# Optimization experiments

Hardware: AMD Instinct MI355X
Metric: run time of the kernel (lower is better)

Reference implementation:

```python
import jax, jax.numpy as jnp
import numpy as np

H, MEL, ATT, TXT = 1024, 80, 640, 640   # n_hidden, n_mel, n_attn_channels, n_text+n_speaker
T, TTXT = 600, 128


def setup_inputs() -> dict:
    key = jax.random.key(0)
    ks = jax.random.split(key, 20)
    def w(k, shape, s=0.02):
        return (jax.random.normal(k, shape) * s).astype(jnp.float32)
    return {
        "residual": jax.random.normal(ks[0], (T, 1, MEL), jnp.float32),
        "text": jax.random.normal(ks[1], (TTXT, 1, TXT), jnp.float32),
        # attention_lstm: LSTM(MEL -> H), 1 layer
        "Wih_a": w(ks[2], (4 * H, MEL)), "Whh_a": w(ks[3], (4 * H, H)),
        "bih_a": jnp.zeros(4 * H, jnp.float32), "bhh_a": jnp.zeros(4 * H, jnp.float32),
        # Attention: query/key/value projections + scoring vector v
        "Wq": w(ks[4], (ATT, H)), "Wk": w(ks[5], (ATT, TXT)), "Wv": w(ks[6], (ATT, TXT)),
        "v_w": w(ks[7], (ATT,)),
        # decoder lstm: LSTM(H+ATT -> H), 2 layers
        "Wih0": w(ks[8], (4 * H, H + ATT)), "Whh0": w(ks[9], (4 * H, H)),
        "bih0": jnp.zeros(4 * H, jnp.float32), "bhh0": jnp.zeros(4 * H, jnp.float32),
        "Wih1": w(ks[10], (4 * H, H)), "Whh1": w(ks[11], (4 * H, H)),
        "bih1": jnp.zeros(4 * H, jnp.float32), "bhh1": jnp.zeros(4 * H, jnp.float32),
        # DenseLayer: two tanh(Linear(H,H))
        "D0w": w(ks[12], (H, H)), "D0b": jnp.zeros(H, jnp.float32),
        "D1w": w(ks[13], (H, H)), "D1b": jnp.zeros(H, jnp.float32),
        # Conv1d(H, 2*MEL, kernel=1) == Linear
        "conv_w": w(ks[14], (2 * MEL, H)), "conv_b": jnp.zeros(2 * MEL, jnp.float32),
        # gate layer: Linear(H+ATT, 1)
        "gate_w": w(ks[15], (H + ATT,)), "gate_b": jnp.zeros((), jnp.float32),
    }


def lstm_cell(x, h, c, Wih, Whh, bih, bhh):
    # PyTorch gate order: i, f, g, o
    g = Wih @ x + bih + Whh @ h + bhh
    i, f, gg, o = jnp.split(g, 4)
    c2 = jax.nn.sigmoid(f) * c + jax.nn.sigmoid(i) * jnp.tanh(gg)
    return jax.nn.sigmoid(o) * jnp.tanh(c2), c2


def ar_back_step(residual, text, Wih_a, Whh_a, bih_a, bhh_a, Wq, Wk, Wv, v_w,
                 Wih0, Whh0, bih0, bhh0, Wih1, Whh1, bih1, bhh1,
                 D0w, D0b, D1w, D1b, conv_w, conv_b, gate_w, gate_b):
    res = residual[::-1, 0, :]            # AR_Back_Step flips time; batch=1 squeezed
    txt = text[:, 0, :]                   # [TTXT, TXT]
    K = txt @ Wk.T                        # [TTXT, ATT]  (keys constant over steps)
    V = txt @ Wv.T                        # [TTXT, ATT]
    z = jnp.zeros(H, jnp.float32)
    carry0 = (jnp.zeros(MEL, jnp.float32), z, z, z, z, z, z)

    def step(carry, r_t):
        out_prev, h, c, h0, c0, h1, c1 = carry
        # attention LSTM on previous output
        h, c = lstm_cell(out_prev, h, c, Wih_a, Whh_a, bih_a, bhh_a)
        # additive (Bahdanau-style) attention: v . tanh(q + K)
        q = Wq @ h                                   # [ATT]
        scores = jnp.tanh(q[None, :] + K) @ v_w      # [TTXT]
        attn = jax.nn.softmax(scores)
        ctx = attn @ V                               # [ATT]
        dec_in = jnp.concatenate([h, ctx])           # [H+ATT]
        # 2-layer decoder LSTM
        h0, c0 = lstm_cell(dec_in, h0, c0, Wih0, Whh0, bih0, bhh0)
        h1, c1 = lstm_cell(h0, h1, c1, Wih1, Whh1, bih1, bhh1)
        # DenseLayer (tanh MLP) then 1x1 conv
        d = jnp.tanh(D1w @ jnp.tanh(D0w @ h1 + D0b) + D1b)
        dec_out = conv_w @ d + conv_b                # [2*MEL]
        log_s, b = dec_out[:MEL], dec_out[MEL:]
        out = (r_t - b) / jnp.exp(log_s)             # affine coupling inverse
        gate = jax.nn.sigmoid(gate_w @ dec_in + gate_b)
        return (out, h, c, h0, c0, h1, c1), (out, gate)

    _, (outs, gates) = jax.lax.scan(step, carry0, res)
    total = outs[::-1][:, None, :]                   # flip back, restore batch dim
    return total, gates


def reference(residual, text, Wih_a, Whh_a, bih_a, bhh_a, Wq, Wk, Wv, v_w,
              Wih0, Whh0, bih0, bhh0, Wih1, Whh1, bih1, bhh1,
              D0w, D0b, D1w, D1b, conv_w, conv_b, gate_w, gate_b):
    return ar_back_step(residual, text, Wih_a, Whh_a, bih_a, bhh_a, Wq, Wk, Wv, v_w,
                        Wih0, Whh0, bih0, bhh0, Wih1, Whh1, bih1, bhh1,
                        D0w, D0b, D1w, D1b, conv_w, conv_b, gate_w, gate_b)
```

## Files before the change

### kernel.cpp

```cpp
#include <hip/hip_runtime.h>

#define NBLK 256
#define NTHR 1024

constexpr int H = 1024, MEL = 80, ATT = 640, TXTD = 640, T = 600, TTXT = 128;
constexpr int G4 = 4096, DIN = H + ATT;

constexpr int WS_K     = 0;
constexpr int WS_V     = WS_K + TTXT * ATT;
constexpr int WS_HV    = WS_V + TTXT * ATT;
constexpr int WS_H0V   = WS_HV + H;
constexpr int WS_H1V   = WS_H0V + H;
constexpr int WS_Q     = WS_H1V + H;
constexpr int WS_SV    = WS_Q + ATT;
constexpr int WS_DEN   = WS_SV + ATT;
constexpr int WS_GH    = WS_DEN + 1;
constexpr int WS_DEC   = (WS_GH + 1 + 15) & ~15;
constexpr int WS_A0    = (WS_DEC + 2 * MEL + 15) & ~15;
constexpr int WS_END   = WS_A0 + H;
constexpr int WS_BAR   = (WS_END + 63) & ~63;

constexpr int SM_W0  = 0;
constexpr int SM_H   = SM_W0 + 16 * DIN;
constexpr int SM_H0  = SM_H + H;
constexpr int SM_H1  = SM_H0 + H;
constexpr int SM_A0  = SM_H1 + H;
constexpr int SM_ATT = SM_A0 + H;
constexpr int SM_K   = SM_ATT + ATT;
constexpr int SM_V   = SM_K + ATT;
constexpr int SM_VW  = SM_V + ATT;
constexpr int SM_OUT = SM_VW + ATT;
constexpr int SM_DEC = SM_OUT + MEL;
constexpr int SM_RED = SM_DEC + 2 * MEL;
constexpr int SM_D   = SM_RED + 16;
constexpr int SM_M   = SM_D + 4;
constexpr int SM_MG  = SM_M + 16 * TTXT;
constexpr int SM_SV  = SM_MG + TTXT;
constexpr int SM_CNT = SM_SV + TTXT;
constexpr size_t SM_BYTES = ((size_t)SM_CNT * 4 + 255) & ~(size_t)255;

#define KEEP4(v) \
  asm volatile("" : "+v"((v).x), "+v"((v).y), "+v"((v).z), "+v"((v).w))

struct Params {
  const float *residual, *text, *Wih_a, *Whh_a, *bih_a, *bhh_a,
      *Wq, *Wk, *Wv, *v_w, *Wih0, *Whh0, *bih0, *bhh0,
      *Wih1, *Whh1, *bih1, *bhh1, *D0w, *D0b, *D1w, *D1b,
      *conv_w, *conv_b, *gate_w, *gate_b;
  float* out;
  float* ws;
};

__device__ __forceinline__ float sigm(float x) { return 1.0f / (1.0f + __expf(-x)); }
__device__ __forceinline__ float ftanh(float x) {
  x = fminf(15.f, fmaxf(-15.f, x));
  float e = __expf(2.f * x);
  return (e - 1.f) / (e + 1.f);
}

__device__ __forceinline__ float aload(const float* p) {
  return __hip_atomic_load(p, __ATOMIC_RELAXED, __HIP_MEMORY_SCOPE_AGENT);
}
__device__ __forceinline__ void astore(float* p, float v) {
  __hip_atomic_store(p, v, __ATOMIC_RELAXED, __HIP_MEMORY_SCOPE_AGENT);
}

__device__ __forceinline__ void g_arrive(unsigned* bar) {
  asm volatile("s_waitcnt vmcnt(0)" ::: "memory");
  __syncthreads();
  if (threadIdx.x == 0) {
    unsigned* leaf = bar + (blockIdx.x & 15) * 32;
    unsigned o = __hip_atomic_fetch_add(leaf, 1u, __ATOMIC_RELAXED,
                                        __HIP_MEMORY_SCOPE_AGENT);
    if ((o & 15) == 15)
      __hip_atomic_fetch_add(bar + 544, 1u, __ATOMIC_RELAXED,
                             __HIP_MEMORY_SCOPE_AGENT);
  }
}
__device__ __forceinline__ void g_wait(unsigned* bar, unsigned target) {
  if (threadIdx.x == 0) {
    while (__hip_atomic_load(bar + 544, __ATOMIC_RELAXED,
                             __HIP_MEMORY_SCOPE_AGENT) < target)
      __builtin_amdgcn_s_sleep(1);
  }
  __syncthreads();
}

__device__ __forceinline__ float red64(float s) {
#pragma unroll
  for (int off = 32; off; off >>= 1) s += __shfl_xor(s, off, 64);
  return s;
}

__device__ __forceinline__ float dot16pin(float4 w0, float4 w1, float4 w2,
                                          float4 w3, const float* x, int lane) {
  const float4* x4 = (const float4*)x;
  float4 b0 = x4[lane], b1 = x4[lane + 64], b2 = x4[lane + 128],
         b3 = x4[lane + 192];
  float s0 = w0.x * b0.x, s1 = w1.x * b1.x;
  s0 = fmaf(w0.y, b0.y, s0); s1 = fmaf(w1.y, b1.y, s1);
  s0 = fmaf(w0.z, b0.z, s0); s1 = fmaf(w1.z, b1.z, s1);
  s0 = fmaf(w0.w, b0.w, s0); s1 = fmaf(w1.w, b1.w, s1);
  s0 = fmaf(w2.x, b2.x, s0); s1 = fmaf(w3.x, b3.x, s1);
  s0 = fmaf(w2.y, b2.y, s0); s1 = fmaf(w3.y, b3.y, s1);
  s0 = fmaf(w2.z, b2.z, s0); s1 = fmaf(w3.z, b3.z, s1);
  s0 = fmaf(w2.w, b2.w, s0); s1 = fmaf(w3.w, b3.w, s1);
  return s0 + s1;
}

__device__ __forceinline__ float dot16load(const float* w, const float* x,
                                           int lane) {
  const float4* w4 = (const float4*)w;
  const float4* x4 = (const float4*)x;
  float4 a0 = w4[lane], a1 = w4[lane + 64], a2 = w4[lane + 128],
         a3 = w4[lane + 192];
  float4 b0 = x4[lane], b1 = x4[lane + 64], b2 = x4[lane + 128],
         b3 = x4[lane + 192];
  float s0 = a0.x * b0.x, s1 = a1.x * b1.x;
  s0 = fmaf(a0.y, b0.y, s0); s1 = fmaf(a1.y, b1.y, s1);
  s0 = fmaf(a0.z, b0.z, s0); s1 = fmaf(a1.z, b1.z, s1);
  s0 = fmaf(a0.w, b0.w, s0); s1 = fmaf(a1.w, b1.w, s1);
  s0 = fmaf(a2.x, b2.x, s0); s1 = fmaf(a3.x, b3.x, s1);
  s0 = fmaf(a2.y, b2.y, s0); s1 = fmaf(a3.y, b3.y, s1);
  s0 = fmaf(a2.z, b2.z, s0); s1 = fmaf(a3.z, b3.z, s1);
  s0 = fmaf(a2.w, b2.w, s0); s1 = fmaf(a3.w, b3.w, s1);
  return s0 + s1;
}

__device__ __forceinline__ float wave_dot(const float* __restrict__ w,
                                          const float* __restrict__ x,
                                          int n4, int lane) {
  float s = 0.f;
  const float4* w4 = (const float4*)w;
  const float4* x4 = (const float4*)x;
  for (int i = lane; i < n4; i += 64) {
    float4 a = w4[i];
    float4 b = x4[i];
    s = fmaf(a.x, b.x, s);
    s = fmaf(a.y, b.y, s);
    s = fmaf(a.z, b.z, s);
    s = fmaf(a.w, b.w, s);
  }
  return red64(s);
}

__global__ void __launch_bounds__(NTHR, 4) ar_kernel(Params p) {
  const int b = blockIdx.x;
  const int tid = threadIdx.x;
  const int wave = tid >> 6;
  const int lane = tid & 63;
  const int sg = wave >> 2;
  const int wg = wave & 3;
  const int gw = b * 16 + wave;

  float* ws = p.ws;
  float* Kw = ws + WS_K;
  float* Vw = ws + WS_V;
  float* hv = ws + WS_HV;
  float* h0v = ws + WS_H0V;
  float* h1v = ws + WS_H1V;
  float* qv = ws + WS_Q;
  float* sv = ws + WS_SV;
  float* ghp = ws + WS_GH;
  float* dec = ws + WS_DEC;
  float* a0g = ws + WS_A0;
  unsigned* bar = (unsigned*)(ws + WS_BAR);

  extern __shared__ __align__(16) float smem[];
  float* s_w0 = smem + SM_W0;
  float* s_h = smem + SM_H;
  float* s_h0 = smem + SM_H0;
  float* s_h1 = smem + SM_H1;
  float* s_a0 = smem + SM_A0;
  float* s_att = smem + SM_ATT;
  float* s_k = smem + SM_K;
  float* s_v = smem + SM_V;
  float* s_vw = smem + SM_VW;
  float* s_out = smem + SM_OUT;
  float* s_dec = smem + SM_DEC;
  float* s_red = smem + SM_RED;
  float* s_d = smem + SM_D;
  float* s_m = smem + SM_M;
  float* s_mg = smem + SM_MG;
  float* s_sv = smem + SM_SV;

  const int e = 4 * b + sg;
  const int grow = e + wg * H;

  const float4* WA = (const float4*)(p.Whh_a + (size_t)grow * H);
  float4 wa0 = WA[lane], wa1 = WA[lane + 64], wa2 = WA[lane + 128],
         wa3 = WA[lane + 192];
  KEEP4(wa0); KEEP4(wa1); KEEP4(wa2); KEEP4(wa3);
  const float4* W0 = (const float4*)(p.Whh0 + (size_t)grow * H);
  float4 w00 = W0[lane], w01 = W0[lane + 64], w02 = W0[lane + 128],
         w03 = W0[lane + 192];
  KEEP4(w00); KEEP4(w01); KEEP4(w02); KEEP4(w03);
  const float4* W1 = (const float4*)(p.Whh1 + (size_t)grow * H);
  float4 w10 = W1[lane], w11 = W1[lane + 64], w12 = W1[lane + 128],
         w13 = W1[lane + 192];
  KEEP4(w10); KEEP4(w11); KEEP4(w12); KEEP4(w13);
  const float4* WI = (const float4*)(p.Wih1 + (size_t)grow * H);
  float4 wi0 = WI[lane], wi1 = WI[lane + 64], wi2 = WI[lane + 128],
         wi3 = WI[lane + 192];
  KEEP4(wi0); KEEP4(wi1); KEEP4(wi2); KEEP4(wi3);
  float4 wma = make_float4(0.f, 0.f, 0.f, 0.f);
  if (lane < MEL / 4)
    wma = ((const float4*)(p.Wih_a + (size_t)grow * MEL))[lane];
  KEEP4(wma);
  float4 wf = ((const float4*)(p.D0w + (size_t)e * H))[wg * 64 + lane];
  KEEP4(wf);
  float4 wgd = ((const float4*)(p.D1w + (size_t)e * H))[wg * 64 + lane];
  KEEP4(wgd);
  float4 wcv = make_float4(0.f, 0.f, 0.f, 0.f);
  if (tid < 2 * MEL) wcv = ((const float4*)(p.conv_w + (size_t)tid * H))[b];
  KEEP4(wcv);
  const float ba = p.bih_a[grow] + p.bhh_a[grow];
  const float b0s = p.bih0[grow] + p.bhh0[grow];
  const float b1s = p.bih1[grow] + p.bhh1[grow];

  const float* xsrc = nullptr;
  if (gw < ATT) xsrc = p.Wq + (size_t)gw * H;
  else if (gw == ATT) xsrc = p.gate_w;

  {
    const float4* src = (const float4*)(p.Wih0 + (size_t)grow * DIN);
    float4* dst = (float4*)(s_w0 + wave * DIN);
    for (int i = lane; i < DIN / 4; i += 64) dst[i] = src[i];
  }
  for (int i = tid; i < ATT; i += NTHR) s_vw[i] = p.v_w[i];
  s_h[tid] = 0.f;
  s_h0[tid] = 0.f;
  s_h1[tid] = 0.f;

  float c_reg = 0.f, c0_reg = 0.f, c1_reg = 0.f;
  float u0_reg = 0.f, u1_reg = 0.f, w0h_reg = 0.f;

  unsigned bk = 0;

  for (int idx = gw; idx < 2 * TTXT * ATT; idx += NBLK * 16) {
    int isV = idx >= TTXT * ATT;
    int rem = isV ? idx - TTXT * ATT : idx;
    int j = rem / ATT;
    int a = rem - j * ATT;
    const float* wrow = (isV ? p.Wv : p.Wk) + a * TXTD;
    float s = wave_dot(wrow, p.text + j * TXTD, TXTD / 4, lane);
    if (lane == 0) astore(&(isV ? Vw : Kw)[j * ATT + a], s);
  }
  g_arrive(bar); ++bk; g_wait(bar, 16 * bk);
  if (b < TTXT) {
    for (int i = tid; i < ATT; i += NTHR) {
      s_k[i] = aload(&Kw[b * ATT + i]);
      s_v[i] = aload(&Vw[b * ATT + i]);
    }
  }
  {
    const float4* wrow = (const float4*)(s_w0 + wave * DIN + H);
    for (int j = 0; j < TTXT; ++j) {
      const float4* v4 = (const float4*)(Vw + j * ATT);
      float s = 0.f;
      for (int i = lane; i < ATT / 4; i += 64) {
        float4 a = wrow[i], x = v4[i];
        s = fmaf(a.x, x.x, s);
        s = fmaf(a.y, x.y, s);
        s = fmaf(a.z, x.z, s);
        s = fmaf(a.w, x.w, s);
      }
      s = red64(s);
      if (lane == 0) s_m[wave * TTXT + j] = s;
    }
  }
  if (b == 0) {
    for (int j = wave; j < TTXT; j += 16) {
      float s = wave_dot(p.gate_w + H, Vw + j * ATT, ATT / 4, lane);
      if (lane == 0) s_mg[j] = s;
    }
  }
  __syncthreads();

  for (int t = 0; t < T; ++t) {
    if (tid < 2 * MEL) s_dec[tid] = aload(dec + tid);
    __syncthreads();
    if (tid < MEL) {
      float o = 0.f;
      if (t != 0) {
        float ls = s_dec[tid] + p.conv_b[tid];
        float bb = s_dec[MEL + tid] + p.conv_b[MEL + tid];
        float r = p.residual[(T - t) * MEL + tid];
        o = (r - bb) * __expf(-ls);
        if (b == 0) p.out[(T - t) * MEL + tid] = o;
      }
      s_out[tid] = o;
    }
    __syncthreads();
    {
      float pa = dot16pin(wa0, wa1, wa2, wa3, s_h, lane);
      if (lane < MEL / 4) {
        float4 bm = ((const float4*)s_out)[lane];
        pa = fmaf(wma.x, bm.x, pa);
        pa = fmaf(wma.y, bm.y, pa);
        pa = fmaf(wma.z, bm.z, pa);
        pa = fmaf(wma.w, bm.w, pa);
      }
      pa = red64(pa);
      if (lane == 0) s_red[wave] = pa + ba;
      __syncthreads();
      if (tid < 4) {
        int ee = 4 * b + tid;
        float gi = s_red[tid * 4 + 0], gf = s_red[tid * 4 + 1];
        float gg = s_red[tid * 4 + 2], go = s_red[tid * 4 + 3];
        float c2 = sigm(gf) * c_reg + sigm(gi) * ftanh(gg);
        c_reg = c2;
        astore(&hv[ee], sigm(go) * ftanh(c2));
      }
    }
    g_arrive(bar); ++bk;
    g_wait(bar, 16 * bk);

    s_h[tid] = aload(hv + tid);
    __syncthreads();
    if (xsrc) {
      float q = dot16load(xsrc, s_h, lane);
      q = red64(q);
      if (lane == 0) {
        if (gw < ATT) astore(&qv[gw], q);
        else astore(&ghp[0], q);
      }
    }
    if (b == NBLK - 1) {
      for (int i = tid; i < 2 * MEL; i += NTHR) astore(&dec[i], 0.f);
    }
    g_arrive(bar); ++bk;
    w0h_reg = red64(dot16load(s_w0 + wave * DIN, s_h, lane));
    g_wait(bar, 16 * bk);

    if (b < TTXT) {
      if (tid < ATT) s_att[tid] = aload(&qv[tid]);
      __syncthreads();
      float sp = 0.f;
      for (int i = tid; i < ATT; i += NTHR)
        sp += ftanh(s_att[i] + s_k[i]) * s_vw[i];
      sp = red64(sp);
      if (lane == 0) s_red[wave] = sp;
      __syncthreads();
      if (tid == 0) {
        float sc = 0.f;
#pragma unroll
        for (int k = 0; k < 16; ++k) sc += s_red[k];
        astore(&sv[b], sc);
      }
    }
    g_arrive(bar); ++bk;
    g_wait(bar, 16 * bk);

    {
      if (tid < TTXT) s_sv[tid] = aload(&sv[tid]);
      __syncthreads();
      float pa_ = __expf(s_sv[lane] - 16.f);
      float pb_ = __expf(s_sv[lane + 64] - 16.f);
      float den_ = red64(pa_ + pb_);
      float w0c = red64(fmaf(pa_, s_m[wave * TTXT + lane],
                             pb_ * s_m[wave * TTXT + lane + 64]));
      if (lane == 0) s_red[wave] = w0c / den_ + w0h_reg + u0_reg + b0s;
      __syncthreads();
      if (tid < 4) {
        int ee = 4 * b + tid;
        float gi = s_red[tid * 4 + 0], gf = s_red[tid * 4 + 1];
        float gg = s_red[tid * 4 + 2], go = s_red[tid * 4 + 3];
        float c2 = sigm(gf) * c0_reg + sigm(gi) * ftanh(gg);
        c0_reg = c2;
        astore(&h0v[ee], sigm(go) * ftanh(c2));
      }
    }
    g_arrive(bar); ++bk;
    if (b == 0 && wave == 15) {
      float pa_ = __expf(s_sv[lane] - 16.f);
      float pb_ = __expf(s_sv[lane + 64] - 16.f);
      float den_ = red64(pa_ + pb_);
      float gc = red64(fmaf(pa_, s_mg[lane], pb_ * s_mg[lane + 64]));
      if (lane == 0) {
        float gh = aload(&ghp[0]);
        p.out[T * MEL + t] = sigm(gh + gc / den_ + p.gate_b[0]);
      }
    }
    g_wait(bar, 16 * bk);

    s_h0[tid] = aload(h0v + tid);
    __syncthreads();
    {
      float pe = dot16pin(wi0, wi1, wi2, wi3, s_h0, lane);
      pe = red64(pe);
      if (lane == 0) s_red[wave] = pe + u1_reg + b1s;
      __syncthreads();
      if (tid < 4) {
        int ee = 4 * b + tid;
        float gi = s_red[tid * 4 + 0], gf = s_red[tid * 4 + 1];
        float gg = s_red[tid * 4 + 2], go = s_red[tid * 4 + 3];
        float c2 = sigm(gf) * c1_reg + sigm(gi) * ftanh(gg);
        c1_reg = c2;
        astore(&h1v[ee], sigm(go) * ftanh(c2));
      }
    }
    g_arrive(bar); ++bk;
    u0_reg = red64(dot16pin(w00, w01, w02, w03, s_h0, lane));
    g_wait(bar, 16 * bk);

    s_h1[tid] = aload(h1v + tid);
    __syncthreads();
    {
      float4 x = ((const float4*)s_h1)[wg * 64 + lane];
      float s = wf.x * x.x;
      s = fmaf(wf.y, x.y, s); s = fmaf(wf.z, x.z, s); s = fmaf(wf.w, x.w, s);
      s = red64(s);
      if (lane == 0) s_red[wave] = s;
      __syncthreads();
      if (tid < 4) {
        int r2 = 4 * b + tid;
        float tot = s_red[tid * 4] + s_red[tid * 4 + 1] + s_red[tid * 4 + 2] +
                    s_red[tid * 4 + 3];
        astore(&a0g[r2], ftanh(tot + p.D0b[r2]));
      }
    }
    g_arrive(bar); ++bk;
    u1_reg = red64(dot16pin(w10, w11, w12, w13, s_h1, lane));
    g_wait(bar, 16 * bk);

    s_a0[tid] = aload(a0g + tid);
    __syncthreads();
    {
      float4 x = ((const float4*)s_a0)[wg * 64 + lane];
      float s = wgd.x * x.x;
      s = fmaf(wgd.y, x.y, s); s = fmaf(wgd.z, x.z, s); s = fmaf(wgd.w, x.w, s);
      s = red64(s);
      if (lane == 0) s_red[wave] = s;
      __syncthreads();
      if (tid < 4) {
        int r2 = 4 * b + tid;
        float tot = s_red[tid * 4] + s_red[tid * 4 + 1] + s_red[tid * 4 + 2] +
                    s_red[tid * 4 + 3];
        s_d[tid] = ftanh(tot + p.D1b[r2]);
      }
      __syncthreads();
      if (tid < 2 * MEL) {
        float acc = wcv.x * s_d[0];
        acc = fmaf(wcv.y, s_d[1], acc);
        acc = fmaf(wcv.z, s_d[2], acc);
        acc = fmaf(wcv.w, s_d[3], acc);
        atomicAdd(&dec[tid], acc);
      }
    }
    g_arrive(bar); ++bk;
    g_wait(bar, 16 * bk);
  }

  if (b == 0 && tid < MEL) {
    float ls = aload(&dec[tid]) + p.conv_b[tid];
    float bb = aload(&dec[MEL + tid]) + p.conv_b[MEL + tid];
    float r = p.residual[tid];
    p.out[tid] = (r - bb) * __expf(-ls);
  }
}

extern "C" void kernel_launch(void* const* d_in, const int* in_sizes, int n_in,
                              void* d_out, int out_size, void* d_ws, size_t ws_size,
                              hipStream_t stream) {
  Params hp;
  hp.residual = (const float*)d_in[0];
  hp.text = (const float*)d_in[1];
  hp.Wih_a = (const float*)d_in[2];
  hp.Whh_a = (const float*)d_in[3];
  hp.bih_a = (const float*)d_in[4];
  hp.bhh_a = (const float*)d_in[5];
  hp.Wq = (const float*)d_in[6];
  hp.Wk = (const float*)d_in[7];
  hp.Wv = (const float*)d_in[8];
  hp.v_w = (const float*)d_in[9];
  hp.Wih0 = (const float*)d_in[10];
  hp.Whh0 = (const float*)d_in[11];
  hp.bih0 = (const float*)d_in[12];
  hp.bhh0 = (const float*)d_in[13];
  hp.Wih1 = (const float*)d_in[14];
  hp.Whh1 = (const float*)d_in[15];
  hp.bih1 = (const float*)d_in[16];
  hp.bhh1 = (const float*)d_in[17];
  hp.D0w = (const float*)d_in[18];
  hp.D0b = (const float*)d_in[19];
  hp.D1w = (const float*)d_in[20];
  hp.D1b = (const float*)d_in[21];
  hp.conv_w = (const float*)d_in[22];
  hp.conv_b = (const float*)d_in[23];
  hp.gate_w = (const float*)d_in[24];
  hp.gate_b = (const float*)d_in[25];
  hp.out = (float*)d_out;
  hp.ws = (float*)d_ws;

  hipMemsetAsync((char*)d_ws + (size_t)WS_BAR * sizeof(float), 0, 4096, stream);

  void* args[] = {&hp};
  hipLaunchCooperativeKernel((void*)ar_kernel, dim3(NBLK), dim3(NTHR), args,
                             (uint32_t)SM_BYTES, stream);
}
```

Before: 25.47 ms.

## Fuse query projection and attention scoring to drop a grid barrier per step

Each of the first 128 blocks now computes five query rows locally and immediately scores all text positions against its slice of K. Partial scores are accumulated with atomics into eight striped buffers, which removes the separate query-to-global exchange and one grid-wide barrier per timestep. The striped buffers are zeroed by the last block later in the step, before they are reused. In exchange it adds atomic traffic, spreads the score sum across blocks, and changes the floating-point summation order.

```diff
diff --git a/kernel.cpp b/kernel.cpp
--- a/kernel.cpp
+++ b/kernel.cpp
@@ -5,16 +5,15 @@
 
 constexpr int H = 1024, MEL = 80, ATT = 640, TXTD = 640, T = 600, TTXT = 128;
 constexpr int G4 = 4096, DIN = H + ATT;
+constexpr int QPB = 5;
 
 constexpr int WS_K     = 0;
 constexpr int WS_V     = WS_K + TTXT * ATT;
 constexpr int WS_HV    = WS_V + TTXT * ATT;
 constexpr int WS_H0V   = WS_HV + H;
 constexpr int WS_H1V   = WS_H0V + H;
-constexpr int WS_Q     = WS_H1V + H;
-constexpr int WS_SV    = WS_Q + ATT;
-constexpr int WS_DEN   = WS_SV + ATT;
-constexpr int WS_GH    = WS_DEN + 1;
+constexpr int WS_SVP   = WS_H1V + H;
+constexpr int WS_GH    = WS_SVP + 8 * TTXT;
 constexpr int WS_DEC   = (WS_GH + 1 + 15) & ~15;
 constexpr int WS_A0    = (WS_DEC + 2 * MEL + 15) & ~15;
 constexpr int WS_END   = WS_A0 + H;
@@ -25,15 +24,14 @@
 constexpr int SM_H0  = SM_H + H;
 constexpr int SM_H1  = SM_H0 + H;
 constexpr int SM_A0  = SM_H1 + H;
-constexpr int SM_ATT = SM_A0 + H;
-constexpr int SM_K   = SM_ATT + ATT;
-constexpr int SM_V   = SM_K + ATT;
-constexpr int SM_VW  = SM_V + ATT;
-constexpr int SM_OUT = SM_VW + ATT;
+constexpr int SM_KT  = SM_A0 + H;
+constexpr int SM_VWL = SM_KT + QPB * TTXT;
+constexpr int SM_QL  = SM_VWL + 8;
+constexpr int SM_OUT = SM_QL + 8;
 constexpr int SM_DEC = SM_OUT + MEL;
 constexpr int SM_RED = SM_DEC + 2 * MEL;
 constexpr int SM_D   = SM_RED + 16;
-constexpr int SM_M   = SM_D + 4;
+constexpr int SM_M   = SM_D + 4 + 8;
 constexpr int SM_MG  = SM_M + 16 * TTXT;
 constexpr int SM_SV  = SM_MG + TTXT;
 constexpr int SM_CNT = SM_SV + TTXT;
@@ -159,8 +157,7 @@
   float* hv = ws + WS_HV;
   float* h0v = ws + WS_H0V;
   float* h1v = ws + WS_H1V;
-  float* qv = ws + WS_Q;
-  float* sv = ws + WS_SV;
+  float* svp = ws + WS_SVP;
   float* ghp = ws + WS_GH;
   float* dec = ws + WS_DEC;
   float* a0g = ws + WS_A0;
@@ -172,10 +169,9 @@
   float* s_h0 = smem + SM_H0;
   float* s_h1 = smem + SM_H1;
   float* s_a0 = smem + SM_A0;
-  float* s_att = smem + SM_ATT;
-  float* s_k = smem + SM_K;
-  float* s_v = smem + SM_V;
-  float* s_vw = smem + SM_VW;
+  float* s_kt = smem + SM_KT;
+  float* s_vwl = smem + SM_VWL;
+  float* s_ql = smem + SM_QL;
   float* s_out = smem + SM_OUT;
   float* s_dec = smem + SM_DEC;
   float* s_red = smem + SM_RED;
@@ -218,16 +214,12 @@
   const float b0s = p.bih0[grow] + p.bhh0[grow];
   const float b1s = p.bih1[grow] + p.bhh1[grow];
 
-  const float* xsrc = nullptr;
-  if (gw < ATT) xsrc = p.Wq + (size_t)gw * H;
-  else if (gw == ATT) xsrc = p.gate_w;
-
   {
     const float4* src = (const float4*)(p.Wih0 + (size_t)grow * DIN);
     float4* dst = (float4*)(s_w0 + wave * DIN);
     for (int i = lane; i < DIN / 4; i += 64) dst[i] = src[i];
   }
-  for (int i = tid; i < ATT; i += NTHR) s_vw[i] = p.v_w[i];
+  if (b < TTXT && tid < QPB) s_vwl[tid] = p.v_w[QPB * b + tid];
   s_h[tid] = 0.f;
   s_h0[tid] = 0.f;
   s_h1[tid] = 0.f;
@@ -246,11 +238,13 @@
     float s = wave_dot(wrow, p.text + j * TXTD, TXTD / 4, lane);
     if (lane == 0) astore(&(isV ? Vw : Kw)[j * ATT + a], s);
   }
+  if (b == 0)
+    for (int i = tid; i < 8 * TTXT; i += NTHR) astore(&svp[i], 0.f);
   g_arrive(bar); ++bk; g_wait(bar, 16 * bk);
   if (b < TTXT) {
-    for (int i = tid; i < ATT; i += NTHR) {
-      s_k[i] = aload(&Kw[b * ATT + i]);
-      s_v[i] = aload(&Vw[b * ATT + i]);
+    for (int i = tid; i < QPB * TTXT; i += NTHR) {
+      int a = i >> 7, d = i & (TTXT - 1);
+      s_kt[i] = aload(&Kw[d * ATT + QPB * b + a]);
     }
   }
   {
@@ -318,42 +312,38 @@
 
     s_h[tid] = aload(hv + tid);
     __syncthreads();
-    if (xsrc) {
-      float q = dot16load(xsrc, s_h, lane);
-      q = red64(q);
-      if (lane == 0) {
-        if (gw < ATT) astore(&qv[gw], q);
-        else astore(&ghp[0], q);
-      }
+    if (b < TTXT && wave < QPB) {
+      float q = red64(
+          dot16load(p.Wq + (size_t)(QPB * b + wave) * H, s_h, lane));
+      if (lane == 0) s_ql[wave] = q;
     }
     if (b == NBLK - 1) {
+      if (wave == 15) {
+        float q = wave_dot(p.gate_w, s_h, H / 4, lane);
+        if (lane == 0) astore(&ghp[0], q);
+      }
       for (int i = tid; i < 2 * MEL; i += NTHR) astore(&dec[i], 0.f);
     }
+    __syncthreads();
+    if (b < TTXT && tid < TTXT) {
+      float partial = 0.f;
+#pragma unroll
+      for (int a = 0; a < QPB; ++a)
+        partial = fmaf(s_vwl[a], ftanh(s_ql[a] + s_kt[a * TTXT + tid]),
+                       partial);
+      atomicAdd(&svp[(b & 7) * TTXT + tid], partial);
+    }
     g_arrive(bar); ++bk;
     w0h_reg = red64(dot16load(s_w0 + wave * DIN, s_h, lane));
     g_wait(bar, 16 * bk);
 
-    if (b < TTXT) {
-      if (tid < ATT) s_att[tid] = aload(&qv[tid]);
-      __syncthreads();
-      float sp = 0.f;
-      for (int i = tid; i < ATT; i += NTHR)
-        sp += ftanh(s_att[i] + s_k[i]) * s_vw[i];
-      sp = red64(sp);
-      if (lane == 0) s_red[wave] = sp;
-      __syncthreads();
-      if (tid == 0) {
-        float sc = 0.f;
+    {
+      if (tid < TTXT) {
+        float s8 = aload(&svp[tid]);
 #pragma unroll
-        for (int k = 0; k < 16; ++k) sc += s_red[k];
-        astore(&sv[b], sc);
-      }
-    }
-    g_arrive(bar); ++bk;
-    g_wait(bar, 16 * bk);
-
-    {
-      if (tid < TTXT) s_sv[tid] = aload(&sv[tid]);
+        for (int g = 1; g < 8; ++g) s8 += aload(&svp[g * TTXT + tid]);
+        s_sv[tid] = s8;
+      }
       __syncthreads();
       float pa_ = __expf(s_sv[lane] - 16.f);
       float pb_ = __expf(s_sv[lane + 64] - 16.f);
@@ -400,6 +390,8 @@
         astore(&h1v[ee], sigm(go) * ftanh(c2));
       }
     }
+    if (b == NBLK - 1 && tid < 8 * TTXT)
+      astore(&svp[tid], 0.f);
     g_arrive(bar); ++bk;
     u0_reg = red64(dot16pin(w00, w01, w02, w03, s_h0, lane));
     g_wait(bar, 16 * bk);
```

New measurement: 23.85 ms. 1.07x faster.
